# Kernel optimization log

Hardware: AMD Instinct MI355X
Metric: run time of the kernel (lower is better)

The kernel has to match this reference:

```python
import jax, jax.numpy as jnp
import numpy as np

N_NODES = 50000
N_EDGES = 800000
N_REL = 16
N_GRAPHS = 64
IN_DIM = 128
HID = 128
FC = 256
N_CLASSES = 16


def setup_inputs() -> dict:
    key = jax.random.key(0)
    ks = jax.random.split(key, 16)
    h = jax.random.normal(ks[0], (N_NODES, IN_DIM), dtype=jnp.float32)
    src = jax.random.randint(ks[1], (N_EDGES,), 0, N_NODES, dtype=jnp.int32)
    dst = jax.random.randint(ks[2], (N_EDGES,), 0, N_NODES, dtype=jnp.int32)
    rel_types = jax.random.randint(ks[3], (N_EDGES,), 0, N_REL, dtype=jnp.int32)
    graph_ids = jnp.sort(jax.random.randint(ks[4], (N_NODES,), 0, N_GRAPHS, dtype=jnp.int32))
    s1 = 1.0 / np.sqrt(IN_DIM)
    s2 = 1.0 / np.sqrt(HID)
    # RGCN layer 1: per-relation weights, self-loop weight, bias
    W1 = jax.random.normal(ks[5], (N_REL, IN_DIM, HID), dtype=jnp.float32) * s1
    Ws1 = jax.random.normal(ks[6], (IN_DIM, HID), dtype=jnp.float32) * s1
    b1 = jnp.zeros((HID,), dtype=jnp.float32)
    # RGCN layer 2
    W2 = jax.random.normal(ks[7], (N_REL, HID, HID), dtype=jnp.float32) * s2
    Ws2 = jax.random.normal(ks[8], (HID, HID), dtype=jnp.float32) * s2
    b2 = jnp.zeros((HID,), dtype=jnp.float32)
    # FC layer after mean pooling
    Wfc = jax.random.normal(ks[9], (HID, FC), dtype=jnp.float32) * s2
    bfc = jnp.zeros((FC,), dtype=jnp.float32)
    # classify head
    Wc = jax.random.normal(ks[10], (FC, N_CLASSES), dtype=jnp.float32) * (1.0 / np.sqrt(FC))
    bc = jnp.zeros((N_CLASSES,), dtype=jnp.float32)
    return dict(h=h, src=src, dst=dst, rel_types=rel_types, graph_ids=graph_ids,
                W1=W1, Ws1=Ws1, b1=b1, W2=W2, Ws2=Ws2, b2=b2,
                Wfc=Wfc, bfc=bfc, Wc=Wc, bc=bc)


def _rel_graph_conv(h, W, Ws, b, src, dst, rel):
    # dgl RelGraphConv (regularizer=None, self_loop=True, bias=True):
    # out[v] = sum_{e:(u->v)} W[rel_e] @ h[u] + Ws @ h[v] + b
    hW = jnp.einsum('ni,rio->rno', h, W)            # [R, N, out]
    msg = hW[rel, src]                               # [E, out] gather per edge
    agg = jax.ops.segment_sum(msg, dst, num_segments=N_NODES)
    return agg + h @ Ws + b


def _mean_nodes(h, graph_ids):
    sums = jax.ops.segment_sum(h, graph_ids, num_segments=N_GRAPHS)      # [G, D]
    cnts = jax.ops.segment_sum(jnp.ones((h.shape[0], 1), h.dtype), graph_ids,
                               num_segments=N_GRAPHS)                    # [G, 1]
    return sums / jnp.maximum(cnts, 1.0)


def reference(h, src, dst, rel_types, graph_ids,
              W1, Ws1, b1, W2, Ws2, b2, Wfc, bfc, Wc, bc):
    h = h.astype(jnp.float32)
    h = jax.nn.relu(_rel_graph_conv(h, W1, Ws1, b1, src, dst, rel_types))
    h = jax.nn.relu(_rel_graph_conv(h, W2, Ws2, b2, src, dst, rel_types))
    hg = _mean_nodes(h, graph_ids)                   # [G, HID]
    hg = jax.nn.relu(hg @ Wfc + bfc)                 # [G, FC]
    return jax.nn.softmax(hg @ Wc + bc, axis=1)      # [G, n_classes]
```

## Files before the change

kernel.cpp:

```cpp
#include <hip/hip_runtime.h>
#include <hip/hip_bf16.h>

#define N_NODES   50000
#define N_PAD     50048
#define N_EDGES   800000
#define N_REL     16
#define N_GRAPHS  64
#define DIM       128
#define FC_DIM    256
#define N_CLASSES 16

#define SB        50176
#define NBINS_P   (16 * SB)
#define NBLK_PP   784
#define NCOARSE   782
#define NCH       392
#define CHSZ      2048
#define NBVIRT    13328
#define GRID_A    1024

#define NBLK_CX   27200
#define XW_TOTAL  (N_PAD * DIM + 2 * 17 * 16384)

#define WS_MARK   0
#define WS_HG     802816
#define WS_CNT    835584
#define WS_SRCOF  835840
#define MEMSET_SZ 4038912
#define WS_BLKH   4038912
#define WS_COFS   5265152
#define WS_PARTP  5268480
#define WS_BLKB   5271808
#define WS_RELB   5275136
#define WS_CIDMAP 5275392
#define WS_RTMP   8486656
#define WS_RECS   11686656
#define WS_OFFSD  14886656
#define WS_X1     15087104
#define WS_X2     27899392
#define WS_WB     40711680
#define WS_T      41825792

typedef __attribute__((ext_vector_type(8))) short bf16x8;
typedef __attribute__((ext_vector_type(4))) float f32x4;

__device__ __forceinline__ void atomAddF(float* p, float v) {
#if defined(__gfx90a__) || defined(__gfx942__) || defined(__gfx950__)
    unsafeAtomicAdd(p, v);
#else
    atomicAdd(p, v);
#endif
}

__device__ __forceinline__ float bf2f(unsigned int u) {
    union { float f; unsigned int i; } x; x.i = u << 16; return x.f;
}
__device__ __forceinline__ unsigned short f2bf(float f) {
    union { float f; unsigned int u; } x; x.f = f;
    unsigned int r = x.u + 0x7fff + ((x.u >> 16) & 1);
    return (unsigned short)(r >> 16);
}
__device__ __forceinline__ void accum8(float* qa, uint4 u) {
    qa[0] += bf2f(u.x & 0xffff); qa[1] += bf2f(u.x >> 16);
    qa[2] += bf2f(u.y & 0xffff); qa[3] += bf2f(u.y >> 16);
    qa[4] += bf2f(u.z & 0xffff); qa[5] += bf2f(u.z >> 16);
    qa[6] += bf2f(u.w & 0xffff); qa[7] += bf2f(u.w >> 16);
}
__device__ __forceinline__ void pack16(const float* qa, unsigned short* dst) {
    #pragma unroll
    for (int j = 0; j < 2; ++j) {
        uint4 w;
        w.x = ((unsigned int)f2bf(qa[j*8+1]) << 16) | f2bf(qa[j*8+0]);
        w.y = ((unsigned int)f2bf(qa[j*8+3]) << 16) | f2bf(qa[j*8+2]);
        w.z = ((unsigned int)f2bf(qa[j*8+5]) << 16) | f2bf(qa[j*8+4]);
        w.w = ((unsigned int)f2bf(qa[j*8+7]) << 16) | f2bf(qa[j*8+6]);
        ((uint4*)dst)[j] = w;
    }
}

__global__ __launch_bounds__(256) void k_h1cx(
    const int* __restrict__ src, const int* __restrict__ dst, const int* __restrict__ rel,
    unsigned char* __restrict__ mark, int* __restrict__ blockHist,
    const float* __restrict__ h, unsigned short* __restrict__ x1,
    const float* __restrict__ W1, const float* __restrict__ Ws1,
    const float* __restrict__ W2, const float* __restrict__ Ws2,
    unsigned short* __restrict__ Wb)
{
    __shared__ int hl[NCOARSE];
    int t = threadIdx.x;
    if (blockIdx.x < NCH) {
        int b = blockIdx.x;
        for (int i = t; i < NCOARSE; i += 256) hl[i] = 0;
        __syncthreads();
        int e0 = b * CHSZ;
        int eend = min(e0 + CHSZ, N_EDGES);
        for (int e = e0 + t; e < eend; e += 256) {
            int d = dst[e];
            mark[rel[e] * SB + src[e]] = 1;
            atomicAdd(&hl[d >> 6], 1);
        }
        __syncthreads();
        for (int i = t; i < NCOARSE; i += 256) blockHist[b * NCOARSE + i] = hl[i];
    } else {
        int id = (blockIdx.x - NCH) * 256 + t;
        if (id < N_PAD * DIM) {
            int v = id >> 7;
            x1[id] = (v < N_NODES) ? f2bf(h[id]) : (unsigned short)0;
        } else {
            int tt = id - N_PAD * DIM;
            int l = tt / 278528, rem = tt % 278528;
            int r = rem >> 14, rr = rem & 16383;
            int n = rr >> 7, k = rr & 127;
            const float* W  = l ? W2 : W1;
            const float* Ws = l ? Ws2 : Ws1;
            float v = (r < 16) ? W[r * 16384 + k * 128 + n] : Ws[k * 128 + n];
            Wb[tt] = f2bf(v);
        }
    }
}

__global__ __launch_bounds__(256) void k_sA(
    const unsigned int* __restrict__ markU, int* __restrict__ partP,
    int* __restrict__ blockHist, int* __restrict__ cOffs)
{
    int t = threadIdx.x;
    if (blockIdx.x < NBLK_PP) {
        __shared__ int red[256];
        int b = blockIdx.x;
        unsigned int u = markU[b * 256 + t];
        red[t] = (int)((u & 1) + ((u >> 8) & 1) + ((u >> 16) & 1) + ((u >> 24) & 1));
        __syncthreads();
        for (int o = 128; o > 0; o >>= 1) {
            if (t < o) red[t] += red[t + o];
            __syncthreads();
        }
        if (t == 0) partP[b] = red[0];
    } else {
        __shared__ int sc[2][256];
        int i = blockIdx.x - NBLK_PP;
        int j0 = 2 * t, j1 = 2 * t + 1;
        int v0 = (j0 < NCH) ? blockHist[j0 * NCOARSE + i] : 0;
        int v1 = (j1 < NCH) ? blockHist[j1 * NCOARSE + i] : 0;
        int p = v0 + v1;
        sc[0][t] = p; __syncthreads();
        int cur = 0;
        for (int o = 1; o < 256; o <<= 1) {
            sc[cur ^ 1][t] = sc[cur][t] + ((t >= o) ? sc[cur][t - o] : 0);
            __syncthreads();
            cur ^= 1;
        }
        int excl = sc[cur][t] - p;
        if (j0 < NCH) blockHist[j0 * NCOARSE + i] = excl;
        if (j1 < NCH) blockHist[j1 * NCOARSE + i] = excl + v0;
        if (t == 255) cOffs[i] = sc[cur][255];
    }
}

__global__ __launch_bounds__(1024) void k_sB(
    const int* __restrict__ partP, int* __restrict__ blkB, int* __restrict__ relB,
    int* __restrict__ cOffs)
{
    int t = threadIdx.x;
    if (blockIdx.x == 0) {
        __shared__ int s1[784], s2[784];
        __shared__ int tot[16], rbase[17];
        int rel = t / 49, pos = t - rel * 49;
        int v = (t < 784) ? partP[t] : 0;
        if (t < 784) s1[t] = v;
        __syncthreads();
        int* cur = s1; int* nxt = s2;
        for (int o = 1; o < 64; o <<= 1) {
            if (t < 784) nxt[t] = cur[t] + ((pos >= o) ? cur[t - o] : 0);
            __syncthreads();
            int* tmp = cur; cur = nxt; nxt = tmp;
        }
        if (t < 784 && pos == 48) tot[rel] = cur[t];
        __syncthreads();
        if (t == 0) {
            int base = 0;
            for (int r = 0; r < 16; ++r) { rbase[r] = base; base += (tot[r] + 63) & ~63; }
            rbase[16] = base;
        }
        __syncthreads();
        if (t < 784) blkB[t] = rbase[rel] + cur[t] - v;
        if (t < 17)  relB[t] = rbase[t];
    } else {
        __shared__ int c1[1024], c2[1024];
        int v = (t < NCOARSE) ? cOffs[t] : 0;
        c1[t] = v; __syncthreads();
        int* cur = c1; int* nxt = c2;
        for (int o = 1; o < 1024; o <<= 1) {
            nxt[t] = cur[t] + ((t >= o) ? cur[t - o] : 0);
            __syncthreads();
            int* tmp = cur; cur = nxt; nxt = tmp;
        }
        if (t < NCOARSE) cOffs[t] = cur[t] - v;
        if (t == NCOARSE) cOffs[NCOARSE] = cur[NCOARSE - 1];
    }
}

__global__ void k_scanPC(const unsigned int* __restrict__ markU, const int* __restrict__ blkB,
                         int* __restrict__ cidMap, int* __restrict__ srcOf) {
    __shared__ int s1[256], s2[256];
    int b = blockIdx.x, t = threadIdx.x;
    unsigned int u = markU[b * 256 + t];
    int f0 = (int)(u & 1), f1 = (int)((u >> 8) & 1);
    int f2 = (int)((u >> 16) & 1), f3 = (int)((u >> 24) & 1);
    int sum = f0 + f1 + f2 + f3;
    s1[t] = sum; __syncthreads();
    int* cur = s1; int* nxt = s2;
    for (int o = 1; o < 256; o <<= 1) {
        nxt[t] = cur[t] + ((t >= o) ? cur[t - o] : 0);
        __syncthreads();
        int* tmp = cur; cur = nxt; nxt = tmp;
    }
    int cid = blkB[b] + cur[t] - sum;
    int rel = b / 49;
    int key0 = b * 1024 + t * 4;
    int srcBase = key0 - rel * SB;
    if (f0) { cidMap[key0]     = cid; srcOf[cid] = srcBase;     cid++; }
    if (f1) { cidMap[key0 + 1] = cid; srcOf[cid] = srcBase + 1; cid++; }
    if (f2) { cidMap[key0 + 2] = cid; srcOf[cid] = srcBase + 2; cid++; }
    if (f3) { cidMap[key0 + 3] = cid; srcOf[cid] = srcBase + 3; cid++; }
}

__global__ __launch_bounds__(256) void k_scat1(
    const int* __restrict__ src, const int* __restrict__ dst, const int* __restrict__ rel,
    const int* __restrict__ cidMap, const int* __restrict__ blockHist,
    const int* __restrict__ cOffs, unsigned int* __restrict__ rtmp)
{
    __shared__ int baseL[NCOARSE];
    __shared__ int hl[NCOARSE];
    int b = blockIdx.x, t = threadIdx.x;
    for (int i = t; i < NCOARSE; i += 256) {
        baseL[i] = blockHist[b * NCOARSE + i] + cOffs[i];
        hl[i] = 0;
    }
    __syncthreads();
    int e0 = b * CHSZ;
    int eend = min(e0 + CHSZ, N_EDGES);
    for (int e = e0 + t; e < eend; e += 256) {
        int d = dst[e];
        int cid = cidMap[rel[e] * SB + src[e]];
        int c = d >> 6;
        int rank = atomicAdd(&hl[c], 1);
        rtmp[baseL[c] + rank] = ((unsigned int)cid << 6) | (unsigned int)(d & 63);
    }
}

__global__ __launch_bounds__(256) void k_p2(
    const unsigned int* __restrict__ rtmp, const int* __restrict__ coarseOffs,
    unsigned int* __restrict__ recs, int* __restrict__ offsD)
{
    __shared__ int cntL[64], exclL[65], cur2[64];
    int i = blockIdx.x, t = threadIdx.x;
    int segB = coarseOffs[i], segE = coarseOffs[i + 1];
    if (t < 64) { cntL[t] = 0; cur2[t] = 0; }
    __syncthreads();
    for (int e = segB + t; e < segE; e += 256)
        atomicAdd(&cntL[rtmp[e] & 63u], 1);
    __syncthreads();
    if (t == 0) {
        int run = segB;
        #pragma unroll
        for (int d = 0; d < 64; ++d) { exclL[d] = run; run += cntL[d]; }
        exclL[64] = run;
    }
    __syncthreads();
    if (t < 64) offsD[i * 64 + t] = exclL[t];
    if (t == 64) offsD[i * 64 + 64] = exclL[64];
    for (int e = segB + t; e < segE; e += 256) {
        unsigned int r = rtmp[e];
        int d = (int)(r & 63u);
        int rank = atomicAdd(&cur2[d], 1);
        recs[exclL[d] + rank] = r >> 6;
    }
}

__global__ __launch_bounds__(256) void k_phaseA(
    const unsigned short* __restrict__ x, const unsigned short* __restrict__ Wb,
    const int* __restrict__ srcOf, const int* __restrict__ relB,
    unsigned short* __restrict__ T)
{
    __shared__ __attribute__((aligned(16))) unsigned short Xs[64 * 136];
    __shared__ __attribute__((aligned(16))) unsigned short Cs[64 * 136];
    __shared__ int sRB[17];

    int tid = threadIdx.x;
    if (tid < 17) sRB[tid] = relB[tid];
    __syncthreads();
    int rtot = sRB[16];

    int row = tid >> 2, c0 = tid & 3;

    auto tileInfo = [&](int vb, int& trow0, int& tr) -> bool {
        int chunk = vb / 136;
        int lane = vb - chunk * 136;
        int r = lane >> 3;
        int i = chunk * 8 + (lane & 7);
        int base, cnt;
        if (r == 16) { base = rtot; cnt = N_PAD / 64; }
        else         { base = sRB[r]; cnt = (sRB[r + 1] - base) >> 6; }
        if (i >= cnt) return false;
        trow0 = base + i * 64; tr = r;
        return true;
    };

    int vb = blockIdx.x;
    int cur_row0, cur_r;
    while (vb < NBVIRT && !tileInfo(vb, cur_row0, cur_r)) vb += gridDim.x;
    if (vb >= NBVIRT) return;

    uint4 g0, g1, g2, g3;
    {
        int sr = (cur_r == 16) ? (cur_row0 - rtot + row) : srcOf[cur_row0 + row];
        const uint4* xp = (const uint4*)(x + (size_t)sr * DIM);
        g0 = xp[c0]; g1 = xp[c0 + 4]; g2 = xp[c0 + 8]; g3 = xp[c0 + 12];
    }

    int w = tid >> 6, l = tid & 63;
    int nl = l & 15, q = l >> 4;

    while (true) {
        {
            uint4* lp = (uint4*)(&Xs[row * 136]);
            lp[c0] = g0; lp[c0 + 4] = g1; lp[c0 + 8] = g2; lp[c0 + 12] = g3;
        }
        bf16x8 Bf[2][4];
        {
            const unsigned short* wr = Wb + cur_r * 16384;
            #pragma unroll
            for (int nt = 0; nt < 2; ++nt) {
                int n = w * 32 + nt * 16 + nl;
                #pragma unroll
                for (int kc = 0; kc < 4; ++kc)
                    Bf[nt][kc] = *(const bf16x8*)(wr + n * 128 + kc * 32 + q * 8);
            }
        }
        int nvb = vb + gridDim.x;
        int nxt_row0 = 0, nxt_r = 0;
        while (nvb < NBVIRT && !tileInfo(nvb, nxt_row0, nxt_r)) nvb += gridDim.x;
        bool nhave = (nvb < NBVIRT);
        if (nhave) {
            int sr = (nxt_r == 16) ? (nxt_row0 - rtot + row) : srcOf[nxt_row0 + row];
            const uint4* xp = (const uint4*)(x + (size_t)sr * DIM);
            g0 = xp[c0]; g1 = xp[c0 + 4]; g2 = xp[c0 + 8]; g3 = xp[c0 + 12];
        }
        __syncthreads();
        #pragma unroll
        for (int m = 0; m < 4; ++m) {
            f32x4 a0 = {0.f, 0.f, 0.f, 0.f}, a1 = {0.f, 0.f, 0.f, 0.f};
            #pragma unroll
            for (int kc = 0; kc < 4; ++kc) {
                bf16x8 a = *(const bf16x8*)(&Xs[(m * 16 + nl) * 136 + kc * 32 + q * 8]);
                a0 = __builtin_amdgcn_mfma_f32_16x16x32_bf16(a, Bf[0][kc], a0, 0, 0, 0);
                a1 = __builtin_amdgcn_mfma_f32_16x16x32_bf16(a, Bf[1][kc], a1, 0, 0, 0);
            }
            int colb = w * 32 + nl;
            #pragma unroll
            for (int reg = 0; reg < 4; ++reg) {
                int row2 = m * 16 + q * 4 + reg;
                int sw = ((row2 >> 3) & 1) << 4;
                Cs[row2 * 136 + (colb ^ sw)]        = f2bf(a0[reg]);
                Cs[row2 * 136 + ((colb + 16) ^ sw)] = f2bf(a1[reg]);
            }
        }
        __syncthreads();
        {
            unsigned short* Tb = T + (size_t)cur_row0 * DIM;
            #pragma unroll
            for (int it = 0; it < 4; ++it) {
                int c = tid + it * 256;
                int rw = c >> 4, k8 = c & 15;
                int sw = ((rw >> 3) & 1) << 4;
                uint4 vv = *(const uint4*)(&Cs[rw * 136 + ((k8 * 8) ^ sw)]);
                *(uint4*)(Tb + rw * DIM + k8 * 8) = vv;
            }
        }
        if (!nhave) break;
        vb = nvb; cur_row0 = nxt_row0; cur_r = nxt_r;
    }
}

__global__ __launch_bounds__(256) void k_phaseB(
    const unsigned short* __restrict__ T, const unsigned int* __restrict__ recs,
    const int* __restrict__ offsD, const int* __restrict__ relB,
    const float* __restrict__ bias,
    unsigned short* __restrict__ aggOut,
    const int* __restrict__ gids, float* __restrict__ hg_sum, int pool)
{
    __shared__ int sOffs[33];
    __shared__ float sBias[128];
    __shared__ int sSelf;
    __shared__ float Sp[32][129];
    __shared__ int sGid[32];
    int tid = threadIdx.x;
    int v0 = blockIdx.x * 32;
    if (tid < 33) sOffs[tid] = offsD[v0 + tid];
    if (tid == 40) sSelf = relB[16];
    if (tid >= 64 && tid < 96) ((float4*)sBias)[tid - 64] = ((const float4*)bias)[tid - 64];
    if (pool && tid < 32) sGid[tid] = (v0 + tid < N_NODES) ? gids[v0 + tid] : -1;
    __syncthreads();

    int g = tid >> 3, s = tid & 7;
    int dst = v0 + g;
    float qa[16];
    #pragma unroll
    for (int i = 0; i < 16; ++i) qa[i] = sBias[s * 16 + i];

    int beg = sOffs[g], end = sOffs[g + 1];
    int e = beg;
    for (; e + 3 < end; e += 4) {
        unsigned int c0 = recs[e], c1 = recs[e+1], c2 = recs[e+2], c3 = recs[e+3];
        const uint4* t0 = (const uint4*)(T + (size_t)c0 * DIM + s * 16);
        const uint4* t1 = (const uint4*)(T + (size_t)c1 * DIM + s * 16);
        const uint4* t2 = (const uint4*)(T + (size_t)c2 * DIM + s * 16);
        const uint4* t3 = (const uint4*)(T + (size_t)c3 * DIM + s * 16);
        uint4 a0 = t0[0], a1 = t0[1], b0 = t1[0], b1 = t1[1];
        uint4 cc0 = t2[0], cc1 = t2[1], d0 = t3[0], d1 = t3[1];
        accum8(qa, a0); accum8(qa + 8, a1);
        accum8(qa, b0); accum8(qa + 8, b1);
        accum8(qa, cc0); accum8(qa + 8, cc1);
        accum8(qa, d0); accum8(qa + 8, d1);
    }
    for (; e < end; ++e) {
        unsigned int c = recs[e];
        const uint4* tp = (const uint4*)(T + (size_t)c * DIM + s * 16);
        uint4 u0 = tp[0], u1 = tp[1];
        accum8(qa, u0); accum8(qa + 8, u1);
    }
    {
        const uint4* tp = (const uint4*)(T + (size_t)(sSelf + dst) * DIM + s * 16);
        uint4 u0 = tp[0], u1 = tp[1];
        accum8(qa, u0); accum8(qa + 8, u1);
    }

    if (!pool) {
        #pragma unroll
        for (int i = 0; i < 16; ++i) qa[i] = fmaxf(qa[i], 0.f);
        pack16(qa, aggOut + (size_t)dst * DIM + s * 16);
    } else {
        #pragma unroll
        for (int i = 0; i < 16; ++i) Sp[g][s * 16 + i] = fmaxf(qa[i], 0.f);
        __syncthreads();
        int d = tid & 127, hh = tid >> 7;
        float run = 0.f; int curg = -2;
        for (int n = hh * 16; n < hh * 16 + 16; ++n) {
            int g2 = sGid[n];
            if (g2 != curg) {
                if (curg >= 0) atomAddF(&hg_sum[curg * DIM + d], run);
                run = 0.f; curg = g2;
            }
            run += Sp[n][d];
        }
        if (curg >= 0) atomAddF(&hg_sum[curg * DIM + d], run);
    }
}

__global__ __launch_bounds__(256) void k_head(
    const float* __restrict__ hg_sum, const int* __restrict__ gids,
    const float* __restrict__ Wfc, const float* __restrict__ bfc,
    const float* __restrict__ Wc, const float* __restrict__ bc,
    float* __restrict__ out)
{
    int g = blockIdx.x, t = threadIdx.x;
    __shared__ float hgl[DIM];
    __shared__ float fcl[FC_DIM];
    __shared__ float lg[N_CLASSES];
    __shared__ int scnt;
    if (t == 0) {
        int lo = 0, hi = N_NODES;
        while (lo < hi) { int mid = (lo + hi) >> 1; if (gids[mid] < g) lo = mid + 1; else hi = mid; }
        int lb = lo;
        hi = N_NODES;
        while (lo < hi) { int mid = (lo + hi) >> 1; if (gids[mid] <= g) lo = mid + 1; else hi = mid; }
        scnt = lo - lb;
    }
    __syncthreads();
    if (t < DIM) {
        float c = (float)max(scnt, 1);
        hgl[t] = hg_sum[g*DIM + t] / c;
    }
    __syncthreads();
    {
        float sv = bfc[t];
        #pragma unroll 4
        for (int k = 0; k < DIM; ++k) sv += hgl[k] * Wfc[k*FC_DIM + t];
        fcl[t] = fmaxf(sv, 0.f);
    }
    __syncthreads();
    if (t < N_CLASSES) {
        float lgt = bc[t];
        #pragma unroll 4
        for (int k = 0; k < FC_DIM; ++k) lgt += fcl[k] * Wc[k*N_CLASSES + t];
        lg[t] = lgt;
    }
    __syncthreads();
    if (t < N_CLASSES) {
        float m = lg[0];
        #pragma unroll
        for (int c = 1; c < N_CLASSES; ++c) m = fmaxf(m, lg[c]);
        float sden = 0.f;
        #pragma unroll
        for (int c = 0; c < N_CLASSES; ++c) sden += expf(lg[c] - m);
        out[g*N_CLASSES + t] = expf(lg[t] - m) / sden;
    }
}

extern "C" void kernel_launch(void* const* d_in, const int* in_sizes, int n_in,
                              void* d_out, int out_size, void* d_ws, size_t ws_size,
                              hipStream_t stream)
{
    const float* h   = (const float*)d_in[0];
    const int*   src = (const int*)d_in[1];
    const int*   dst = (const int*)d_in[2];
    const int*   rel = (const int*)d_in[3];
    const int*   gid = (const int*)d_in[4];
    const float* W1  = (const float*)d_in[5];
    const float* Ws1 = (const float*)d_in[6];
    const float* b1  = (const float*)d_in[7];
    const float* W2  = (const float*)d_in[8];
    const float* Ws2 = (const float*)d_in[9];
    const float* b2  = (const float*)d_in[10];
    const float* Wfc = (const float*)d_in[11];
    const float* bfc = (const float*)d_in[12];
    const float* Wc  = (const float*)d_in[13];
    const float* bc  = (const float*)d_in[14];
    float* out = (float*)d_out;

    char* ws = (char*)d_ws;
    unsigned char* mark = (unsigned char*)(ws + WS_MARK);
    float* hgsum = (float*)(ws + WS_HG);
    int*   srcOf = (int*)(ws + WS_SRCOF);
    int*   blkH  = (int*)(ws + WS_BLKH);
    int*   cOffs = (int*)(ws + WS_COFS);
    int*   partP = (int*)(ws + WS_PARTP);
    int*   blkB  = (int*)(ws + WS_BLKB);
    int*   relB  = (int*)(ws + WS_RELB);
    int*   cidMap= (int*)(ws + WS_CIDMAP);
    unsigned int* rtmp = (unsigned int*)(ws + WS_RTMP);
    unsigned int* recs = (unsigned int*)(ws + WS_RECS);
    int*   offsD = (int*)(ws + WS_OFFSD);
    unsigned short* x1  = (unsigned short*)(ws + WS_X1);
    unsigned short* x2  = (unsigned short*)(ws + WS_X2);
    unsigned short* Wb  = (unsigned short*)(ws + WS_WB);
    unsigned short* T   = (unsigned short*)(ws + WS_T);

    hipMemsetAsync(mark, 0, MEMSET_SZ, stream);

    k_h1cx<<<NCH + NBLK_CX, 256, 0, stream>>>(src, dst, rel, mark, blkH,
                                              h, x1, W1, Ws1, W2, Ws2, Wb);
    k_sA<<<NBLK_PP + NCOARSE, 256, 0, stream>>>((const unsigned int*)mark, partP,
                                                blkH, cOffs);
    k_sB<<<2, 1024, 0, stream>>>(partP, blkB, relB, cOffs);
    k_scanPC<<<NBLK_PP, 256, 0, stream>>>((const unsigned int*)mark, blkB, cidMap, srcOf);

    k_scat1<<<NCH, 256, 0, stream>>>(src, dst, rel, cidMap, blkH, cOffs, rtmp);
    k_p2<<<NCOARSE, 256, 0, stream>>>(rtmp, cOffs, recs, offsD);

    k_phaseA<<<GRID_A, 256, 0, stream>>>(x1, Wb, srcOf, relB, T);
    k_phaseB<<<N_PAD / 32, 256, 0, stream>>>(T, recs, offsD, relB, b1, x2, gid, hgsum, 0);
    k_phaseA<<<GRID_A, 256, 0, stream>>>(x2, Wb + 17 * 16384, srcOf, relB, T);
    k_phaseB<<<N_PAD / 32, 256, 0, stream>>>(T, recs, offsD, relB, b2, x2, gid, hgsum, 1);

    k_head<<<N_GRAPHS, 256, 0, stream>>>(hgsum, gid, Wfc, bfc, Wc, bc, out);
}
```

Before: 377.0 us.

## Co-schedule edge scatter passes with layer-1 transform GEMM in shared launches

Merges the two edge-sorting kernels (scatter to coarse bins, fine per-destination sort) with the layer-1 per-relation transform kernel. Each fused launch gives its first blocks the sorting work and its remaining blocks half of the virtual GEMM tiles, so the independent passes overlap and two launch boundaries go away. The sort scratch reuses the GEMM's shared memory. The tile range split is fixed, so imbalance between the aux blocks and the GEMM blocks could leave CUs idle.

New measurement: 382.4 us. Within noise of the previous version (+1.4%).

```diff
diff --git a/kernel.cpp b/kernel.cpp
--- a/kernel.cpp
+++ b/kernel.cpp
@@ -17,7 +17,8 @@
 #define NCH       392
 #define CHSZ      2048
 #define NBVIRT    13328
-#define GRID_A    1024
+#define VB_SPLIT  6664
+#define PA_BLK    1024
 
 #define NBLK_CX   27200
 #define XW_TOTAL  (N_PAD * DIM + 2 * 17 * 16384)
@@ -224,69 +225,74 @@
     if (f3) { cidMap[key0 + 3] = cid; srcOf[cid] = srcBase + 3; cid++; }
 }
 
-__global__ __launch_bounds__(256) void k_scat1(
+__global__ __launch_bounds__(256) void k_fuseAP(
+    const unsigned short* __restrict__ x, const unsigned short* __restrict__ Wb,
+    const int* __restrict__ srcOf, const int* __restrict__ relB,
+    unsigned short* __restrict__ T,
     const int* __restrict__ src, const int* __restrict__ dst, const int* __restrict__ rel,
     const int* __restrict__ cidMap, const int* __restrict__ blockHist,
-    const int* __restrict__ cOffs, unsigned int* __restrict__ rtmp)
-{
-    __shared__ int baseL[NCOARSE];
-    __shared__ int hl[NCOARSE];
-    int b = blockIdx.x, t = threadIdx.x;
-    for (int i = t; i < NCOARSE; i += 256) {
-        baseL[i] = blockHist[b * NCOARSE + i] + cOffs[i];
-        hl[i] = 0;
-    }
-    __syncthreads();
-    int e0 = b * CHSZ;
-    int eend = min(e0 + CHSZ, N_EDGES);
-    for (int e = e0 + t; e < eend; e += 256) {
-        int d = dst[e];
-        int cid = cidMap[rel[e] * SB + src[e]];
-        int c = d >> 6;
-        int rank = atomicAdd(&hl[c], 1);
-        rtmp[baseL[c] + rank] = ((unsigned int)cid << 6) | (unsigned int)(d & 63);
-    }
-}
-
-__global__ __launch_bounds__(256) void k_p2(
-    const unsigned int* __restrict__ rtmp, const int* __restrict__ coarseOffs,
-    unsigned int* __restrict__ recs, int* __restrict__ offsD)
-{
-    __shared__ int cntL[64], exclL[65], cur2[64];
-    int i = blockIdx.x, t = threadIdx.x;
-    int segB = coarseOffs[i], segE = coarseOffs[i + 1];
-    if (t < 64) { cntL[t] = 0; cur2[t] = 0; }
-    __syncthreads();
-    for (int e = segB + t; e < segE; e += 256)
-        atomicAdd(&cntL[rtmp[e] & 63u], 1);
-    __syncthreads();
-    if (t == 0) {
-        int run = segB;
-        #pragma unroll
-        for (int d = 0; d < 64; ++d) { exclL[d] = run; run += cntL[d]; }
-        exclL[64] = run;
-    }
-    __syncthreads();
-    if (t < 64) offsD[i * 64 + t] = exclL[t];
-    if (t == 64) offsD[i * 64 + 64] = exclL[64];
-    for (int e = segB + t; e < segE; e += 256) {
-        unsigned int r = rtmp[e];
-        int d = (int)(r & 63u);
-        int rank = atomicAdd(&cur2[d], 1);
-        recs[exclL[d] + rank] = r >> 6;
-    }
-}
-
-__global__ __launch_bounds__(256) void k_phaseA(
-    const unsigned short* __restrict__ x, const unsigned short* __restrict__ Wb,
-    const int* __restrict__ srcOf, const int* __restrict__ relB,
-    unsigned short* __restrict__ T)
+    const int* __restrict__ cOffs, unsigned int* __restrict__ rtmp,
+    unsigned int* __restrict__ recs, int* __restrict__ offsD,
+    int mode, int auxN, int vb0, int vb1)
 {
     __shared__ __attribute__((aligned(16))) unsigned short Xs[64 * 136];
     __shared__ __attribute__((aligned(16))) unsigned short Cs[64 * 136];
     __shared__ int sRB[17];
 
     int tid = threadIdx.x;
+
+    if ((int)blockIdx.x < auxN) {
+        if (mode == 1) {
+            int* baseL = (int*)Xs;
+            int* hl    = ((int*)Xs) + NCOARSE;
+            int b = blockIdx.x;
+            for (int i = tid; i < NCOARSE; i += 256) {
+                baseL[i] = blockHist[b * NCOARSE + i] + cOffs[i];
+                hl[i] = 0;
+            }
+            __syncthreads();
+            int e0 = b * CHSZ;
+            int eend = min(e0 + CHSZ, N_EDGES);
+            for (int e = e0 + tid; e < eend; e += 256) {
+                int d = dst[e];
+                int cid = cidMap[rel[e] * SB + src[e]];
+                int c = d >> 6;
+                int rank = atomicAdd(&hl[c], 1);
+                rtmp[baseL[c] + rank] = ((unsigned int)cid << 6) | (unsigned int)(d & 63);
+            }
+        } else {
+            int* cntL  = (int*)Xs;
+            int* exclL = ((int*)Xs) + 64;
+            int* cur2  = ((int*)Xs) + 129;
+            int i = blockIdx.x;
+            int segB = cOffs[i], segE = cOffs[i + 1];
+            if (tid < 64) { cntL[tid] = 0; cur2[tid] = 0; }
+            __syncthreads();
+            for (int e = segB + tid; e < segE; e += 256)
+                atomicAdd(&cntL[rtmp[e] & 63u], 1);
+            __syncthreads();
+            if (tid == 0) {
+                int run = segB;
+                #pragma unroll
+                for (int d = 0; d < 64; ++d) { exclL[d] = run; run += cntL[d]; }
+                exclL[64] = run;
+            }
+            __syncthreads();
+            if (tid < 64) offsD[i * 64 + tid] = exclL[tid];
+            if (tid == 64) offsD[i * 64 + 64] = exclL[64];
+            for (int e = segB + tid; e < segE; e += 256) {
+                unsigned int r = rtmp[e];
+                int d = (int)(r & 63u);
+                int rank = atomicAdd(&cur2[d], 1);
+                recs[exclL[d] + rank] = r >> 6;
+            }
+        }
+        return;
+    }
+
+    int paBid = (int)blockIdx.x - auxN;
+    int paStride = (int)gridDim.x - auxN;
+
     if (tid < 17) sRB[tid] = relB[tid];
     __syncthreads();
     int rtot = sRB[16];
@@ -306,10 +312,10 @@
         return true;
     };
 
-    int vb = blockIdx.x;
+    int vb = vb0 + paBid;
     int cur_row0, cur_r;
-    while (vb < NBVIRT && !tileInfo(vb, cur_row0, cur_r)) vb += gridDim.x;
-    if (vb >= NBVIRT) return;
+    while (vb < vb1 && !tileInfo(vb, cur_row0, cur_r)) vb += paStride;
+    if (vb >= vb1) return;
 
     uint4 g0, g1, g2, g3;
     {
@@ -337,10 +343,10 @@
                     Bf[nt][kc] = *(const bf16x8*)(wr + n * 128 + kc * 32 + q * 8);
             }
         }
-        int nvb = vb + gridDim.x;
+        int nvb = vb + paStride;
         int nxt_row0 = 0, nxt_r = 0;
-        while (nvb < NBVIRT && !tileInfo(nvb, nxt_row0, nxt_r)) nvb += gridDim.x;
-        bool nhave = (nvb < NBVIRT);
+        while (nvb < vb1 && !tileInfo(nvb, nxt_row0, nxt_r)) nvb += paStride;
+        bool nhave = (nvb < vb1);
         if (nhave) {
             int sr = (nxt_r == 16) ? (nxt_row0 - rtot + row) : srcOf[nxt_row0 + row];
             const uint4* xp = (const uint4*)(x + (size_t)sr * DIM);
@@ -555,12 +561,19 @@
     k_sB<<<2, 1024, 0, stream>>>(partP, blkB, relB, cOffs);
     k_scanPC<<<NBLK_PP, 256, 0, stream>>>((const unsigned int*)mark, blkB, cidMap, srcOf);
 
-    k_scat1<<<NCH, 256, 0, stream>>>(src, dst, rel, cidMap, blkH, cOffs, rtmp);
-    k_p2<<<NCOARSE, 256, 0, stream>>>(rtmp, cOffs, recs, offsD);
-
-    k_phaseA<<<GRID_A, 256, 0, stream>>>(x1, Wb, srcOf, relB, T);
+    k_fuseAP<<<NCH + PA_BLK, 256, 0, stream>>>(x1, Wb, srcOf, relB, T,
+                                               src, dst, rel, cidMap, blkH, cOffs,
+                                               rtmp, recs, offsD,
+                                               1, NCH, 0, VB_SPLIT);
+    k_fuseAP<<<NCOARSE + PA_BLK, 256, 0, stream>>>(x1, Wb, srcOf, relB, T,
+                                                   src, dst, rel, cidMap, blkH, cOffs,
+                                                   rtmp, recs, offsD,
+                                                   2, NCOARSE, VB_SPLIT, NBVIRT);
     k_phaseB<<<N_PAD / 32, 256, 0, stream>>>(T, recs, offsD, relB, b1, x2, gid, hgsum, 0);
-    k_phaseA<<<GRID_A, 256, 0, stream>>>(x2, Wb + 17 * 16384, srcOf, relB, T);
+    k_fuseAP<<<PA_BLK, 256, 0, stream>>>(x2, Wb + 17 * 16384, srcOf, relB, T,
+                                         src, dst, rel, cidMap, blkH, cOffs,
+                                         rtmp, recs, offsD,
+                                         0, 0, 0, NBVIRT);
     k_phaseB<<<N_PAD / 32, 256, 0, stream>>>(T, recs, offsD, relB, b2, x2, gid, hgsum, 1);
 
     k_head<<<N_GRAPHS, 256, 0, stream>>>(hgsum, gid, Wfc, bfc, Wc, bc, out);
```
